# Performance work log

Hardware: AMD Instinct MI355X
Metric: run time of the kernel (lower is better)

## Reference

```python
import jax, jax.numpy as jnp
import numpy as np

N = 2000      # batch_size * num_rois
PS = 7        # pool_size
C = 256       # roi-align channels
HID = 1024    # head width
NC = 81       # num_classes (COCO incl. background)
EPS = 1e-3    # keras BatchNormalization default epsilon


def setup_inputs() -> dict:
    key = jax.random.key(0)
    ks = jax.random.split(key, 6)
    sc = lambda k, shape, s: jax.random.normal(k, shape, jnp.float32) * s
    return {
        "pooled_rois": jax.random.normal(ks[0], (N, PS, PS, C), jnp.float32),
        # 7x7 VALID conv on a 7x7 input == flattened dense: [PS*PS*C, HID]
        "w1": sc(ks[1], (PS * PS * C, HID), 0.01),
        "b1": jnp.zeros((HID,), jnp.float32),
        "gamma1": jnp.ones((HID,), jnp.float32),
        "beta1": jnp.zeros((HID,), jnp.float32),
        # 1x1 conv == dense [HID, HID]
        "w2": sc(ks[2], (HID, HID), 0.02),
        "b2": jnp.zeros((HID,), jnp.float32),
        "gamma2": jnp.ones((HID,), jnp.float32),
        "beta2": jnp.zeros((HID,), jnp.float32),
        "w_logits": sc(ks[3], (HID, NC), 0.02),
        "b_logits": jnp.zeros((NC,), jnp.float32),
        "w_delta": sc(ks[4], (HID, NC * 4), 0.02),
        "b_delta": jnp.zeros((NC * 4,), jnp.float32),
    }


def _batchnorm_train(x, gamma, beta):
    # training=True: normalize with batch statistics over the RoI axis
    mu = jnp.mean(x, axis=0)
    var = jnp.var(x, axis=0)
    return gamma * (x - mu) * jax.lax.rsqrt(var + EPS) + beta


def reference(pooled_rois, w1, b1, gamma1, beta1, w2, b2, gamma2, beta2,
              w_logits, b_logits, w_delta, b_delta):
    n = pooled_rois.shape[0]
    # rcnn_class_conv1: 7x7 VALID conv on 7x7 input -> flatten + matmul
    x = pooled_rois.reshape(n, -1) @ w1 + b1          # [N, 1024]
    x = jax.nn.relu(_batchnorm_train(x, gamma1, beta1))
    # rcnn_class_conv2: 1x1 conv -> matmul
    x = x @ w2 + b2                                    # [N, 1024]
    x = jax.nn.relu(_batchnorm_train(x, gamma2, beta2))
    logits = x @ w_logits + b_logits                   # [N, NC]
    probs = jax.nn.softmax(logits, axis=-1)            # [N, NC]
    deltas = (x @ w_delta + b_delta).reshape(n, NC, 4) # [N, NC, 4]
    return logits, probs, deltas
```

## Files before the change

kernel.cpp:

```cpp
#include <hip/hip_runtime.h>

typedef unsigned short u16;
typedef __bf16 bf16x8 __attribute__((ext_vector_type(8)));
typedef float f32x4 __attribute__((ext_vector_type(4)));
typedef u16 u16x8 __attribute__((ext_vector_type(8)));

static constexpr int kNRoi = 2000;
static constexpr int kMPad = 2048;
static constexpr int kKin  = 12544;
static constexpr int kHid  = 1024;
static constexpr int kNOutPad = 512;
static constexpr int kNC = 81;
static constexpr int kND = 324;


__device__ __forceinline__ u16 f2bf(float f) {
  union { float f; unsigned u; } v; v.f = f;
  unsigned r = v.u + 0x7fffu + ((v.u >> 16) & 1u);
  return (u16)(r >> 16);
}

__device__ __forceinline__ void transpose64(const float* __restrict__ in,
                                            u16* __restrict__ out, int R, int C,
                                            int bx, int by, u16* t, int tid) {
  const int cb = bx * 64, rb = by * 64;
  const int rl = tid >> 4, cl = (tid & 15) * 4;
#pragma unroll
  for (int i = 0; i < 4; ++i) {
    int r = rl + i * 16;
    f32x4 v = *(const f32x4*)(in + (long)(rb + r) * C + cb + cl);
#pragma unroll
    for (int j = 0; j < 4; ++j) t[(cl + j) * 72 + r] = f2bf(v[j]);
  }
  __syncthreads();
  const int c2 = tid >> 3, r2 = (tid & 7) * 8;
#pragma unroll
  for (int i = 0; i < 2; ++i) {
    int c = c2 + i * 32;
    u16x8 v = *(const u16x8*)&t[c * 72 + r2];
    *(u16x8*)(out + (long)(cb + c) * R + rb + r2) = v;
  }
}

__device__ __forceinline__ void transpose32(const float* __restrict__ in,
                                            u16* __restrict__ out, int R, int C,
                                            int bx, int by, u16* t, int tid) {
  int tx = tid & 31, ty = tid >> 5;
  int cb = bx * 32, rb = by * 32;
#pragma unroll
  for (int i = 0; i < 4; ++i) {
    int r = rb + ty + i * 8, c = cb + tx;
    if (r < R && c < C) t[(ty + i * 8) * 33 + tx] = f2bf(in[(long)r * C + c]);
  }
  __syncthreads();
#pragma unroll
  for (int i = 0; i < 4; ++i) {
    int c = cb + ty + i * 8, r = rb + tx;
    if (c < C && r < R) out[(long)c * R + r] = t[tx * 33 + ty + i * 8];
  }
}

__global__ __launch_bounds__(256) void prep(
    const float* __restrict__ pooled, const float* __restrict__ w1,
    const float* __restrict__ w2, const float* __restrict__ wl,
    const float* __restrict__ wd, u16* __restrict__ A1,
    u16* __restrict__ W1T, u16* __restrict__ W2T, u16* __restrict__ WHT,
    float* __restrict__ X1, float* __restrict__ S) {
  __shared__ u16 sh[64 * 72];
  const int tid = threadIdx.x;
  int id = blockIdx.x;
  if (id < 12250) {
    long i = ((long)id * 256 + tid) * 8;
    f32x4 a = *(const f32x4*)(pooled + i);
    f32x4 b = *(const f32x4*)(pooled + i + 4);
    u16x8 h;
#pragma unroll
    for (int j = 0; j < 4; ++j) { h[j] = f2bf(a[j]); h[4 + j] = f2bf(b[j]); }
    *(u16x8*)(A1 + i) = h;
    return;
  }
  id -= 12250;
  if (id < 3136) { transpose64(w1, W1T, kKin, kHid, id & 15, id >> 4, sh, tid); return; }
  id -= 3136;
  if (id < 256)  { transpose64(w2, W2T, kHid, kHid, id & 15, id >> 4, sh, tid); return; }
  id -= 256;
  if (id < 96)   { transpose32(wl, WHT, kHid, kNC, id % 3, id / 3, sh, tid); return; }
  id -= 96;
  if (id < 352)  { transpose32(wd, WHT + kNC * kHid, kHid, kND, id % 11, id / 11, sh, tid); return; }
  id -= 352;
  if (id < 54) {
    int idx = id * 256 + tid;
    if (idx < 13696) *(u16x8*)(WHT + 405 * kHid + idx * 8) = (u16x8){};
    return;
  }
  id -= 54;
  if (id < 2048) {
    *(f32x4*)(X1 + ((long)id * 256 + tid) * 4) = (f32x4){};
    return;
  }
  id -= 2048;
  *(f32x4*)(S + ((long)id * 256 + tid) * 4) = (f32x4){};
}

__global__ __launch_bounds__(256) void gemm_bt(
    const u16* __restrict__ A, const u16* __restrict__ Bt,
    float* __restrict__ C, int Mreal, int K, int N, int kchunk) {
  __shared__ u16 As[2][128 * 32];
  __shared__ u16 Bs[2][128 * 32];
  const int tid  = threadIdx.x;
  const int lane = tid & 63;
  const int wave = tid >> 6;
  const int wm = (wave >> 1) * 64;
  const int wn = (wave & 1) * 64;

  f32x4 acc[4][4] = {};

  const int r0 = tid >> 2;
  const int kc = (tid & 3) * 8;
  long ar0 = (long)blockIdx.x * 128 + r0;      if (ar0 > Mreal - 1) ar0 = Mreal - 1;
  long ar1 = (long)blockIdx.x * 128 + 64 + r0; if (ar1 > Mreal - 1) ar1 = Mreal - 1;
  const long br0 = (long)blockIdx.y * 128 + r0;
  const long br1 = br0 + 64;

  const int kb = blockIdx.z * kchunk;
  const u16* ag0 = A + ar0 * K + kb + kc;
  const u16* ag1 = A + ar1 * K + kb + kc;
  const u16* bg0 = Bt + br0 * K + kb + kc;
  const u16* bg1 = Bt + br1 * K + kb + kc;

  const int fr = lane & 15;
  const int fq = (lane >> 4) * 8;
  const int iters = kchunk / 32;

#define STAGE(b) do {                                                          \
    u16* al_ = As[b] + wave * 512;                                             \
    u16* bl_ = Bs[b] + wave * 512;                                             \
    __builtin_amdgcn_global_load_lds((const __attribute__((address_space(1))) void*)ag0, \
                                     (__attribute__((address_space(3))) void*)al_, 16, 0, 0); \
    __builtin_amdgcn_global_load_lds((const __attribute__((address_space(1))) void*)ag1, \
                                     (__attribute__((address_space(3))) void*)(al_ + 2048), 16, 0, 0); \
    __builtin_amdgcn_global_load_lds((const __attribute__((address_space(1))) void*)bg0, \
                                     (__attribute__((address_space(3))) void*)bl_, 16, 0, 0); \
    __builtin_amdgcn_global_load_lds((const __attribute__((address_space(1))) void*)bg1, \
                                     (__attribute__((address_space(3))) void*)(bl_ + 2048), 16, 0, 0); \
    ag0 += 32; ag1 += 32; bg0 += 32; bg1 += 32;                                \
  } while (0)

  STAGE(0);
  int buf = 0;
  for (int it = 0; it < iters; ++it) {
    __syncthreads();
    if (it + 1 < iters) STAGE(buf ^ 1);

    const u16* as_ = As[buf];
    const u16* bs_ = Bs[buf];
    bf16x8 afr[4], bfr[4];
#pragma unroll
    for (int i = 0; i < 4; ++i)
      afr[i] = *(const bf16x8*)(as_ + (wm + i * 16 + fr) * 32 + fq);
#pragma unroll
    for (int i = 0; i < 4; ++i)
      bfr[i] = *(const bf16x8*)(bs_ + (wn + i * 16 + fr) * 32 + fq);
#pragma unroll
    for (int mi = 0; mi < 4; ++mi)
#pragma unroll
      for (int ni = 0; ni < 4; ++ni)
        acc[mi][ni] = __builtin_amdgcn_mfma_f32_16x16x32_bf16(afr[mi], bfr[ni], acc[mi][ni], 0, 0, 0);
    buf ^= 1;
  }
#undef STAGE

  const int row0 = blockIdx.x * 128 + wm + (lane >> 4) * 4;
  const int col0 = blockIdx.y * 128 + wn + fr;
#pragma unroll
  for (int mi = 0; mi < 4; ++mi)
#pragma unroll
    for (int ni = 0; ni < 4; ++ni)
#pragma unroll
      for (int e = 0; e < 4; ++e)
        atomicAdd(&C[(long)(row0 + mi * 16 + e) * N + col0 + ni * 16], acc[mi][ni][e]);
}

__global__ __launch_bounds__(256) void colstats_zero(
    const float* __restrict__ X, float* __restrict__ S, float* __restrict__ SS,
    float* __restrict__ Z) {
  int id = blockIdx.x;
  if (id < 320) {
    int c = (id & 3) * 256 + threadIdx.x;
    int r0 = (id >> 2) * 25;
    float s = 0.f, ss = 0.f;
    for (int r = r0; r < r0 + 25; ++r) {
      float v = X[(long)r * kHid + c];
      s += v; ss += v * v;
    }
    atomicAdd(&S[c], s);
    atomicAdd(&SS[c], ss);
  } else {
    id -= 320;
    *(f32x4*)(Z + ((long)id * 256 + threadIdx.x) * 4) = (f32x4){};
  }
}

__global__ __launch_bounds__(256) void bn_relu(
    const float* __restrict__ X, const float* __restrict__ S,
    const float* __restrict__ SS, const float* __restrict__ gamma,
    const float* __restrict__ beta, u16* __restrict__ H) {
  constexpr float invN = 1.f / (float)kNRoi;
  long i = ((long)blockIdx.x * 256 + threadIdx.x) * 8;
  int c = (int)(i & (kHid - 1));
  f32x4 x0 = *(const f32x4*)(X + i);
  f32x4 x1 = *(const f32x4*)(X + i + 4);
  f32x4 s0 = *(const f32x4*)(S + c),    s1 = *(const f32x4*)(S + c + 4);
  f32x4 q0 = *(const f32x4*)(SS + c),   q1 = *(const f32x4*)(SS + c + 4);
  f32x4 g0 = *(const f32x4*)(gamma + c), g1 = *(const f32x4*)(gamma + c + 4);
  f32x4 b0 = *(const f32x4*)(beta + c),  b1 = *(const f32x4*)(beta + c + 4);
  u16x8 h;
#pragma unroll
  for (int j = 0; j < 4; ++j) {
    float mu = s0[j] * invN;
    float var = q0[j] * invN - mu * mu;
    float sc = g0[j] * rsqrtf(var + 1e-3f);
    h[j] = f2bf(fmaxf(0.f, sc * x0[j] + (b0[j] - mu * sc)));
    mu = s1[j] * invN;
    var = q1[j] * invN - mu * mu;
    sc = g1[j] * rsqrtf(var + 1e-3f);
    h[4 + j] = f2bf(fmaxf(0.f, sc * x1[j] + (b1[j] - mu * sc)));
  }
  *(u16x8*)(H + i) = h;
}

__global__ __launch_bounds__(256) void head_out(
    const float* __restrict__ X, const float* __restrict__ bl,
    const float* __restrict__ bd, float* __restrict__ out) {
  int lane = threadIdx.x & 63;
  int row = blockIdx.x * 4 + (threadIdx.x >> 6);
  if (row >= kNRoi) return;
  const float* xr = X + (long)row * kNOutPad;
  float v0 = xr[lane] + bl[lane];
  float v1 = (lane < kNC - 64) ? xr[64 + lane] + bl[64 + lane] : -3.0e38f;
  float m = fmaxf(v0, v1);
#pragma unroll
  for (int off = 32; off > 0; off >>= 1) m = fmaxf(m, __shfl_xor(m, off, 64));
  float e0 = __expf(v0 - m);
  float e1 = (lane < kNC - 64) ? __expf(v1 - m) : 0.f;
  float s = e0 + e1;
#pragma unroll
  for (int off = 32; off > 0; off >>= 1) s += __shfl_xor(s, off, 64);
  float inv = 1.f / s;
  float* lo = out + (long)row * kNC;
  float* pr = out + (long)kNRoi * kNC + (long)row * kNC;
  float* de = out + 2L * kNRoi * kNC + (long)row * kND;
  lo[lane] = v0;
  pr[lane] = e0 * inv;
  if (lane < kNC - 64) { lo[64 + lane] = v1; pr[64 + lane] = e1 * inv; }
#pragma unroll
  for (int j = 0; j < 5; ++j) {
    int c = lane + 64 * j;
    de[c] = xr[kNC + c] + bd[c];
  }
  if (lane < 4) { int c = lane + 320; de[c] = xr[kNC + c] + bd[c]; }
}

extern "C" void kernel_launch(void* const* d_in, const int* in_sizes, int n_in,
                              void* d_out, int out_size, void* d_ws, size_t ws_size,
                              hipStream_t stream) {
  const float* pooled   = (const float*)d_in[0];
  const float* w1       = (const float*)d_in[1];
  const float* gamma1   = (const float*)d_in[3];
  const float* beta1    = (const float*)d_in[4];
  const float* w2       = (const float*)d_in[5];
  const float* gamma2   = (const float*)d_in[7];
  const float* beta2    = (const float*)d_in[8];
  const float* w_logits = (const float*)d_in[9];
  const float* b_logits = (const float*)d_in[10];
  const float* w_delta  = (const float*)d_in[11];
  const float* b_delta  = (const float*)d_in[12];

  char* ws = (char*)d_ws;
  u16*   W1T  = (u16*)(ws + 0);
  u16*   W2T  = (u16*)(ws + 25690112);
  u16*   WHT  = (u16*)(ws + 27787264);
  float* X1   = (float*)(ws + 28835840);
  u16*   H    = (u16*)(ws + 37224448);
  float* S    = (float*)(ws + 41418752);
  u16*   A1   = (u16*)(ws + 41435136);
  float* X2   = (float*)(ws + 41435136);
  float* XOUT = (float*)(ws + 49823744);

  float* S1  = S;
  float* SS1 = S + 1024;
  float* S2  = S + 2048;
  float* SS2 = S + 3072;

  prep<<<18196, 256, 0, stream>>>(pooled, w1, w2, w_logits, w_delta,
                                  A1, W1T, W2T, WHT, X1, S);

  gemm_bt<<<dim3(16, 8, 8), 256, 0, stream>>>(A1, W1T, X1, kNRoi, kKin, kHid, kKin / 8);

  colstats_zero<<<320 + 3072, 256, 0, stream>>>(X1, S1, SS1, X2);
  bn_relu<<<(kMPad * kHid) / 2048, 256, 0, stream>>>(X1, S1, SS1, gamma1, beta1, H);

  gemm_bt<<<dim3(16, 8, 4), 256, 0, stream>>>(H, W2T, X2, kMPad, kHid, kHid, kHid / 4);

  colstats_zero<<<320, 256, 0, stream>>>(X2, S2, SS2, nullptr);
  bn_relu<<<(kMPad * kHid) / 2048, 256, 0, stream>>>(X2, S2, SS2, gamma2, beta2, H);

  gemm_bt<<<dim3(16, 4, 4), 256, 0, stream>>>(H, WHT, XOUT, kMPad, kHid, kNOutPad, kHid / 4);

  head_out<<<kNRoi / 4, 256, 0, stream>>>(XOUT, b_logits, b_delta, (float*)d_out);
}
```

Measured before the change: 387.6 us.

## Fuse fp32-to-bf16 activation conversion into first GEMM's LDS load path

Drops the separate prep pass that converted pooled RoIs from fp32 to a bf16 buffer. A new GEMM kernel reads fp32 activations straight into LDS via global_load_lds with an XOR swizzle and converts them to bf16 when building MFMA fragments. This avoids writing and re-reading a ~50MB intermediate. In exchange it doubles LDS traffic and footprint for A, adds per-iteration conversion work, and since each A tile is re-read by 8 column blocks, fp32 global reads for A double.

```diff
diff --git a/kernel.cpp b/kernel.cpp
--- a/kernel.cpp
+++ b/kernel.cpp
@@ -20,6 +20,13 @@
   return (u16)(r >> 16);
 }
 
+__device__ __forceinline__ bf16x8 cvt8(f32x4 lo, f32x4 hi) {
+  bf16x8 r;
+#pragma unroll
+  for (int j = 0; j < 4; ++j) { r[j] = (__bf16)lo[j]; r[4 + j] = (__bf16)hi[j]; }
+  return r;
+}
+
 __device__ __forceinline__ void transpose64(const float* __restrict__ in,
                                             u16* __restrict__ out, int R, int C,
                                             int bx, int by, u16* t, int tid) {
@@ -61,25 +68,13 @@
 }
 
 __global__ __launch_bounds__(256) void prep(
-    const float* __restrict__ pooled, const float* __restrict__ w1,
-    const float* __restrict__ w2, const float* __restrict__ wl,
-    const float* __restrict__ wd, u16* __restrict__ A1,
+    const float* __restrict__ w1, const float* __restrict__ w2,
+    const float* __restrict__ wl, const float* __restrict__ wd,
     u16* __restrict__ W1T, u16* __restrict__ W2T, u16* __restrict__ WHT,
     float* __restrict__ X1, float* __restrict__ S) {
   __shared__ u16 sh[64 * 72];
   const int tid = threadIdx.x;
   int id = blockIdx.x;
-  if (id < 12250) {
-    long i = ((long)id * 256 + tid) * 8;
-    f32x4 a = *(const f32x4*)(pooled + i);
-    f32x4 b = *(const f32x4*)(pooled + i + 4);
-    u16x8 h;
-#pragma unroll
-    for (int j = 0; j < 4; ++j) { h[j] = f2bf(a[j]); h[4 + j] = f2bf(b[j]); }
-    *(u16x8*)(A1 + i) = h;
-    return;
-  }
-  id -= 12250;
   if (id < 3136) { transpose64(w1, W1T, kKin, kHid, id & 15, id >> 4, sh, tid); return; }
   id -= 3136;
   if (id < 256)  { transpose64(w2, W2T, kHid, kHid, id & 15, id >> 4, sh, tid); return; }
@@ -100,6 +95,98 @@
   }
   id -= 2048;
   *(f32x4*)(S + ((long)id * 256 + tid) * 4) = (f32x4){};
+}
+
+__global__ __launch_bounds__(256) void gemm1_f32a(
+    const float* __restrict__ A, const u16* __restrict__ Bt,
+    float* __restrict__ C, int Mreal, int K, int N, int kchunk) {
+  __shared__ float As[2][4096];
+  __shared__ u16   Bs[2][4096];
+  const int tid  = threadIdx.x;
+  const int lane = tid & 63;
+  const int wave = tid >> 6;
+  const int wm = (wave >> 1) * 64;
+  const int wn = (wave & 1) * 64;
+
+  f32x4 acc[4][4] = {};
+
+  const int kb = blockIdx.z * kchunk;
+
+  const int dr   = lane >> 3;
+  const int jsrc = (lane & 7) ^ dr;
+  const float* pA[4];
+#pragma unroll
+  for (int i = 0; i < 4; ++i) {
+    long r = (long)blockIdx.x * 128 + 32 * i + 8 * wave + dr;
+    if (r > Mreal - 1) r = Mreal - 1;
+    pA[i] = A + r * K + kb + jsrc * 4;
+  }
+
+  const int r0 = tid >> 2;
+  const int kc = (tid & 3) * 8;
+  const long br0 = (long)blockIdx.y * 128 + r0;
+  const u16* bg0 = Bt + br0 * K + kb + kc;
+  const u16* bg1 = Bt + (br0 + 64) * K + kb + kc;
+
+  const int fr = lane & 15;
+  const int fq = (lane >> 4) * 8;
+  const int j0 = (lane >> 4) * 2;
+  const int iters = kchunk / 32;
+
+#define STAGE(b) do {                                                          \
+    _Pragma("unroll")                                                          \
+    for (int i_ = 0; i_ < 4; ++i_) {                                           \
+      __builtin_amdgcn_global_load_lds(                                        \
+        (const __attribute__((address_space(1))) void*)pA[i_],                 \
+        (__attribute__((address_space(3))) void*)&As[b][(i_ * 256 + wave * 64) * 4], 16, 0, 0); \
+      pA[i_] += 32;                                                            \
+    }                                                                          \
+    u16* bl_ = Bs[b] + wave * 512;                                             \
+    __builtin_amdgcn_global_load_lds((const __attribute__((address_space(1))) void*)bg0, \
+                                     (__attribute__((address_space(3))) void*)bl_, 16, 0, 0); \
+    __builtin_amdgcn_global_load_lds((const __attribute__((address_space(1))) void*)bg1, \
+                                     (__attribute__((address_space(3))) void*)(bl_ + 2048), 16, 0, 0); \
+    bg0 += 32; bg1 += 32;                                                      \
+  } while (0)
+
+  STAGE(0);
+  int buf = 0;
+  for (int it = 0; it < iters; ++it) {
+    __syncthreads();
+    if (it + 1 < iters) STAGE(buf ^ 1);
+
+    const float* as_ = As[buf];
+    const u16*   bs_ = Bs[buf];
+    bf16x8 afr[4], bfr[4];
+#pragma unroll
+    for (int i = 0; i < 4; ++i) {
+      int r = wm + i * 16 + fr;
+      int g0 = r * 8 + (j0 ^ (fr & 7));
+      f32x4 lo = *(const f32x4*)(as_ + g0 * 4);
+      f32x4 hi = *(const f32x4*)(as_ + (g0 ^ 1) * 4);
+      afr[i] = cvt8(lo, hi);
+    }
+#pragma unroll
+    for (int i = 0; i < 4; ++i)
+      bfr[i] = *(const bf16x8*)(bs_ + (wn + i * 16 + fr) * 32 + fq);
+#pragma unroll
+    for (int mi = 0; mi < 4; ++mi)
+#pragma unroll
+      for (int ni = 0; ni < 4; ++ni)
+        acc[mi][ni] = __builtin_amdgcn_mfma_f32_16x16x32_bf16(afr[mi], bfr[ni], acc[mi][ni], 0, 0, 0);
+    buf ^= 1;
+  }
+#undef STAGE
+
+  const int row0 = blockIdx.x * 128 + wm + (lane >> 4) * 4;
+  const int col0 = blockIdx.y * 128 + wn + fr;
+#pragma unroll
+  for (int mi = 0; mi < 4; ++mi)
+#pragma unroll
+    for (int ni = 0; ni < 4; ++ni)
+#pragma unroll
+      for (int e = 0; e < 4; ++e)
+        atomicAdd(&C[(long)(row0 + mi * 16 + e) * N + col0 + ni * 16], acc[mi][ni][e]);
 }
 
 __global__ __launch_bounds__(256) void gemm_bt(
@@ -283,7 +370,6 @@
   float* X1   = (float*)(ws + 28835840);
   u16*   H    = (u16*)(ws + 37224448);
   float* S    = (float*)(ws + 41418752);
-  u16*   A1   = (u16*)(ws + 41435136);
   float* X2   = (float*)(ws + 41435136);
   float* XOUT = (float*)(ws + 49823744);
 
@@ -292,10 +378,9 @@
   float* S2  = S + 2048;
   float* SS2 = S + 3072;
 
-  prep<<<18196, 256, 0, stream>>>(pooled, w1, w2, w_logits, w_delta,
-                                  A1, W1T, W2T, WHT, X1, S);
-
-  gemm_bt<<<dim3(16, 8, 8), 256, 0, stream>>>(A1, W1T, X1, kNRoi, kKin, kHid, kKin / 8);
+  prep<<<5946, 256, 0, stream>>>(w1, w2, w_logits, w_delta, W1T, W2T, WHT, X1, S);
+
+  gemm1_f32a<<<dim3(16, 8, 8), 256, 0, stream>>>(pooled, W1T, X1, kNRoi, kKin, kHid, kKin / 8);
 
   colstats_zero<<<320 + 3072, 256, 0, stream>>>(X1, S1, SS1, X2);
   bn_relu<<<(kMPad * kHid) / 2048, 256, 0, stream>>>(X1, S1, SS1, gamma1, beta1, H);
```

After: 414.9 us. 1.07x slower.
